# Kernel optimization log

Measured on AMD Instinct MI355X. Metric: run time of the kernel, lower is better.

## Reference

```python
import jax, jax.numpy as jnp
import numpy as np

N_HEAD = 16


def _rope_cos_sin(T, head_dim, dtype):
    inv_freq = 1.0 / (10000.0 ** (jnp.arange(0, head_dim, 2, dtype=jnp.float32) / head_dim))
    t = jnp.arange(T, dtype=jnp.float32)
    freqs = jnp.outer(t, inv_freq)  # [T, head_dim//2]
    return jnp.cos(freqs).astype(dtype), jnp.sin(freqs).astype(dtype)


def _apply_rope(x, cos, sin):
    # x: [B, H, T, D]; cos/sin: [T, D//2]
    x_even = x[..., ::2]
    x_odd = x[..., 1::2]
    c = cos[None, None, :, :]
    s = sin[None, None, :, :]
    out_even = x_even * c - x_odd * s
    out_odd = x_even * s + x_odd * c
    # interleave back: [..., D//2, 2] -> [..., D]
    return jnp.stack((out_even, out_odd), axis=-1).reshape(x.shape)


def setup_inputs() -> dict:
    key = jax.random.key(0)
    k1, k2, k3 = jax.random.split(key, 3)
    B, T, C = 2, 2048, 1024
    x = jax.random.normal(k1, (B, T, C), dtype=jnp.float32)
    w_qkv = jax.random.normal(k2, (C, 3 * C), dtype=jnp.float32) * (1.0 / np.sqrt(C))
    w_proj = jax.random.normal(k3, (C, C), dtype=jnp.float32) * (1.0 / np.sqrt(C))
    b_proj = jnp.zeros((C,), dtype=jnp.float32)
    return {"x": x, "w_qkv": w_qkv, "w_proj": w_proj, "b_proj": b_proj}


def reference(x, w_qkv, w_proj, b_proj):
    B, T, C = x.shape
    H = N_HEAD
    D = C // H
    qkv = x @ w_qkv  # [B, T, 3C]
    q, k, v = jnp.split(qkv, 3, axis=2)
    # [B, T, C] -> [B, H, T, D]
    q = q.reshape(B, T, H, D).transpose(0, 2, 1, 3)
    k = k.reshape(B, T, H, D).transpose(0, 2, 1, 3)
    v = v.reshape(B, T, H, D).transpose(0, 2, 1, 3)
    cos, sin = _rope_cos_sin(T, D, q.dtype)
    q = _apply_rope(q, cos, sin)
    k = _apply_rope(k, cos, sin)
    # causal SDPA
    scale = 1.0 / np.sqrt(D)
    att = jnp.einsum('bhqd,bhkd->bhqk', q, k) * scale
    causal = jnp.tril(jnp.ones((T, T), dtype=bool))
    att = jnp.where(causal[None, None, :, :], att, jnp.finfo(att.dtype).min)
    att = jax.nn.softmax(att, axis=-1)
    y = jnp.einsum('bhqk,bhkd->bhqd', att, v)  # [B, H, T, D]
    y = y.transpose(0, 2, 1, 3).reshape(B, T, C)
    return y @ w_proj + b_proj
```

## Files before the change

### kernel.cpp

```cpp
#include <hip/hip_runtime.h>
#include <math.h>

#define T_SEQ 2048
#define CDIM  1024
#define HEADS 16
#define DHEAD 64
#define BATCH 2
#define M_ROWS 4096
#define QSCALE 0.18033688011112042f

typedef unsigned short u16;
typedef unsigned int u32;
typedef __attribute__((ext_vector_type(8))) short bf16x8;
typedef __attribute__((ext_vector_type(4))) float f32x4;
typedef __attribute__((ext_vector_type(16))) float f32x16;

__device__ inline u16 f2bf(float f) {
    u32 u = __builtin_bit_cast(u32, f);
    u32 r = (u + 0x7fffu + ((u >> 16) & 1u)) >> 16;
    return (u16)r;
}

__device__ inline u32 cvtpk(float lo, float hi) {
    u32 r;
    asm("v_cvt_pk_bf16_f32 %0, %1, %2" : "=v"(r) : "v"(lo), "v"(hi));
    return r;
}

__device__ inline void permswap(u32& x, u32& y) {
    asm volatile("v_permlane32_swap_b32 %0, %1" : "+v"(x), "+v"(y));
}

__device__ inline float fexp2(float x) {
#if __has_builtin(__builtin_amdgcn_exp2f)
    return __builtin_amdgcn_exp2f(x);
#else
    float r; asm("v_exp_f32 %0, %1" : "=v"(r) : "v"(x)); return r;
#endif
}

__device__ inline void gload16(const void* g, void* l) {
    __builtin_amdgcn_global_load_lds(
        (const __attribute__((address_space(1))) void*)g,
        (__attribute__((address_space(3))) void*)l, 16, 0, 0);
}

__global__ void rope_table_kernel(float* __restrict__ cosT, float* __restrict__ sinT) {
    int idx = blockIdx.x * blockDim.x + threadIdx.x;
    if (idx >= T_SEQ * 32) return;
    int t = idx >> 5;
    int i = idx & 31;
    float expo = (2.0f * (float)i) / 64.0f;
    float inv = powf(10000.0f, -expo);
    float a = (float)t * inv;
    cosT[idx] = cosf(a);
    sinT[idx] = sinf(a);
}

__global__ __launch_bounds__(256)
void conv_bf16(const float* __restrict__ in, u16* __restrict__ out, int n8) {
    int i = blockIdx.x * blockDim.x + threadIdx.x;
    if (i >= n8) return;
    const float4* p = (const float4*)(in + (size_t)i * 8);
    float4 a = p[0], b = p[1];
    uint4 o;
    o.x = (u32)f2bf(a.x) | ((u32)f2bf(a.y) << 16);
    o.y = (u32)f2bf(a.z) | ((u32)f2bf(a.w) << 16);
    o.z = (u32)f2bf(b.x) | ((u32)f2bf(b.y) << 16);
    o.w = (u32)f2bf(b.z) | ((u32)f2bf(b.w) << 16);
    *(uint4*)(out + (size_t)i * 8) = o;
}

__global__ __launch_bounds__(256)
void convT64(const float* __restrict__ in, u16* __restrict__ out, int K, int N) {
    __shared__ float Ls[64][65];
    const int tid = threadIdx.x;
    const int k0 = blockIdx.y << 6, n0 = blockIdx.x << 6;
    const int r0 = tid >> 4, c4 = (tid & 15) << 2;
#pragma unroll
    for (int p = 0; p < 4; p++) {
        int r = r0 + (p << 4);
        float4 v = *(const float4*)&in[(size_t)(k0 + r) * N + n0 + c4];
        Ls[r][c4 + 0] = v.x; Ls[r][c4 + 1] = v.y;
        Ls[r][c4 + 2] = v.z; Ls[r][c4 + 3] = v.w;
    }
    __syncthreads();
    const int n = tid >> 2, kq = (tid & 3) << 4;
    u32 pk[8];
#pragma unroll
    for (int j = 0; j < 8; j++) {
        float lo = Ls[kq + 2 * j][n], hi = Ls[kq + 2 * j + 1][n];
        pk[j] = (u32)f2bf(lo) | ((u32)f2bf(hi) << 16);
    }
    u32* dst = (u32*)&out[(size_t)(n0 + n) * K + k0 + kq];
    ((uint4*)dst)[0] = make_uint4(pk[0], pk[1], pk[2], pk[3]);
    ((uint4*)dst)[1] = make_uint4(pk[4], pk[5], pk[6], pk[7]);
}

__global__ __launch_bounds__(256)
void transposeV(const u16* __restrict__ in, u16* __restrict__ out) {
    __shared__ u16 Ls[64][72];
    const int tid = threadIdx.x;
    const int bh = blockIdx.y;
    const int t0 = blockIdx.x << 6;
    const u16* src = in + ((size_t)bh << 17) + ((size_t)t0 << 6);
#pragma unroll
    for (int p = 0; p < 2; p++) {
        int L = tid + (p << 8);
        int t = L >> 3, c = L & 7;
        uint4 v = *(const uint4*)&src[(size_t)t * 64 + (c << 3)];
        *(uint4*)&Ls[t][c << 3] = v;
    }
    __syncthreads();
    const int d = tid >> 2, tq = (tid & 3) << 4;
    u32 pk[8];
#pragma unroll
    for (int j = 0; j < 8; j++) {
        u16 lo = Ls[tq + 2 * j][d], hi = Ls[tq + 2 * j + 1][d];
        pk[j] = (u32)lo | ((u32)hi << 16);
    }
    u16* dst = out + ((size_t)bh << 17) + ((size_t)d << 11) + t0 + tq;
    ((uint4*)dst)[0] = make_uint4(pk[0], pk[1], pk[2], pk[3]);
    ((uint4*)dst)[1] = make_uint4(pk[4], pk[5], pk[6], pk[7]);
}

template <int EPI>
__global__ __launch_bounds__(256)
void gemm_bf16(const u16* __restrict__ A, const u16* __restrict__ Bt,
               int N, int K,
               const float* __restrict__ bias, float* __restrict__ outF,
               u16* __restrict__ qOut, u16* __restrict__ kOut, u16* __restrict__ vOut,
               const float* __restrict__ cosT, const float* __restrict__ sinT) {
    __shared__ u16 Alds[2][128 * 32];
    __shared__ u16 Blds[2][128 * 32];
    const int tid = threadIdx.x;
    const int lane = tid & 63;
    const int w = tid >> 6;
    const int wr = w >> 1, wc = w & 1;
    const int g = lane >> 4, l15 = lane & 15;
    const int m0 = blockIdx.y * 128, n0 = blockIdx.x * 128;

    f32x4 acc[4][4];
#pragma unroll
    for (int m = 0; m < 4; m++)
#pragma unroll
        for (int n = 0; n < 4; n++)
#pragma unroll
            for (int e = 0; e < 4; e++) acc[m][n][e] = 0.f;

    int aoff[4], boff[4];
#pragma unroll
    for (int m = 0; m < 4; m++) {
        aoff[m] = ((wr << 6) + (m << 4) + l15) * 64 + (g << 4);
        boff[m] = ((wc << 6) + (m << 4) + l15) * 64 + (g << 4);
    }
    const int rowA0 = tid >> 2, kk0 = (tid & 3) << 3;

#define GSTAGE(BUF, K0)                                                          \
    {                                                                            \
        _Pragma("unroll") for (int pq = 0; pq < 2; pq++) {                       \
            int L = tid + (pq << 8);                                             \
            int row = rowA0 + (pq << 6);                                         \
            gload16(A + (size_t)(m0 + row) * K + (K0) + kk0, &Alds[BUF][0] + L * 8); \
            gload16(Bt + (size_t)(n0 + row) * K + (K0) + kk0, &Blds[BUF][0] + L * 8); \
        }                                                                        \
    }

    GSTAGE(0, 0);
    const int nt = K >> 5;
    int cur = 0;
    for (int t = 0; t < nt; t++) {
        if (t + 1 < nt) {
            GSTAGE(cur ^ 1, ((t + 1) << 5));
            asm volatile("s_waitcnt vmcnt(4)" ::: "memory");
        } else {
            asm volatile("s_waitcnt vmcnt(0)" ::: "memory");
        }
        __builtin_amdgcn_s_barrier();
        asm volatile("" ::: "memory");
        bf16x8 af[4], bfr[4];
#pragma unroll
        for (int m = 0; m < 4; m++) af[m] = *(const bf16x8*)((const char*)&Alds[cur][0] + aoff[m]);
#pragma unroll
        for (int n = 0; n < 4; n++) bfr[n] = *(const bf16x8*)((const char*)&Blds[cur][0] + boff[n]);
#pragma unroll
        for (int m = 0; m < 4; m++)
#pragma unroll
            for (int n = 0; n < 4; n++)
                acc[m][n] = __builtin_amdgcn_mfma_f32_16x16x32_bf16(af[m], bfr[n], acc[m][n], 0, 0, 0);
        asm volatile("" ::: "memory");
        __builtin_amdgcn_s_barrier();
        cur ^= 1;
    }
#undef GSTAGE

    if (EPI == 0) {
        const int sec = n0 >> 10;
#pragma unroll
        for (int m = 0; m < 4; m++) {
#pragma unroll
            for (int j = 0; j < 4; j++) {
                int t = m0 + (wr << 6) + (m << 4) + (g << 2) + j;
                int b = t >> 11, tt = t & 2047;
#pragma unroll
                for (int n = 0; n < 4; n++) {
                    int cc = (n0 + (wc << 6) + (n << 4) + l15) & 1023;
                    int h = cc >> 6, d = cc & 63;
                    float val = acc[m][n][j];
                    float o = val;
                    if (sec < 2) {
                        float partner = __shfl_xor(val, 1);
                        int i0 = d >> 1;
                        float c = cosT[tt * 32 + i0], s = sinT[tt * 32 + i0];
                        o = ((d & 1) == 0) ? (val * c - partner * s)
                                           : (partner * s + val * c);
                        if (sec == 0) o *= QSCALE;
                    }
                    size_t off = (((size_t)((b * 16 + h) * 2048 + tt)) << 6) + d;
                    u16* dst = (sec == 0) ? qOut : ((sec == 1) ? kOut : vOut);
                    dst[off] = f2bf(o);
                }
            }
        }
    } else {
#pragma unroll
        for (int m = 0; m < 4; m++) {
#pragma unroll
            for (int j = 0; j < 4; j++) {
                int t = m0 + (wr << 6) + (m << 4) + (g << 2) + j;
#pragma unroll
                for (int n = 0; n < 4; n++) {
                    int col = n0 + (wc << 6) + (n << 4) + l15;
                    outF[(size_t)t * N + col] = acc[m][n][j] + bias[col];
                }
            }
        }
    }
}

__device__ __forceinline__ void kv_stage2(const u16* Kb, const u16* Vtb,
                                          u16* Kl, u16* Vl, int tid, int k0) {
#pragma unroll
    for (int pp = 0; pp < 2; pp++) {
        int L = tid + (pp << 8);
        int row = L >> 3, c = L & 7;
        int cg = (c ^ (row & 7)) << 3;
        gload16(Kb + (((size_t)(k0 + row)) << 6) + cg, Kl + L * 8);
        gload16(Vtb + ((size_t)row << 11) + k0 + cg, Vl + L * 8);
    }
}

template <bool MASKED>
__device__ __forceinline__ void attn_step32(
    const bf16x8 (&qf)[4], f32x16 (&O)[2], float& MR, float& LR,
    const char* Kl, const char* Vl, const int (&foff)[2][4], int lim) {
    f32x16 st[2];
    __builtin_amdgcn_s_setprio(1);
#pragma unroll
    for (int s = 0; s < 2; s++) {
#pragma unroll
        for (int e = 0; e < 16; e++) st[s][e] = 0.f;
#pragma unroll
        for (int ks = 0; ks < 4; ks++) {
            bf16x8 kf = *(const bf16x8*)(Kl + foff[s][ks]);
            st[s] = __builtin_amdgcn_mfma_f32_32x32x16_bf16(kf, qf[ks], st[s], 0, 0, 0);
        }
    }
    __builtin_amdgcn_s_setprio(0);
    if (MASKED) {
#pragma unroll
        for (int s = 0; s < 2; s++) {
            const int ls = lim - (s << 5);
#pragma unroll
            for (int r = 0; r < 16; r++) {
                const int kvloc = (r & 3) + 8 * (r >> 2);
                if (kvloc > ls) st[s][r] = -1e30f;
            }
        }
    }
    float t8[8];
#pragma unroll
    for (int r = 0; r < 8; r++)
        t8[r] = fmaxf(fmaxf(st[0][r], st[0][r + 8]),
                      fmaxf(st[1][r], st[1][r + 8]));
    float m = fmaxf(fmaxf(fmaxf(t8[0], t8[4]), fmaxf(t8[1], t8[5])),
                    fmaxf(fmaxf(t8[2], t8[6]), fmaxf(t8[3], t8[7])));
    m = fmaxf(m, __shfl_xor(m, 32));
    float mn = fmaxf(MR, m);
    if (__ballot(m - MR > 10.f)) {
        float al = fexp2(MR - mn);
        MR = mn;
        LR *= al;
#pragma unroll
        for (int e = 0; e < 16; e++) { O[0][e] *= al; O[1][e] *= al; }
    }
    float s0 = 0.f, s1 = 0.f, s2 = 0.f, s3 = 0.f;
#pragma unroll
    for (int s = 0; s < 2; s++)
#pragma unroll
        for (int r = 0; r < 16; r++) {
            float pv = fexp2(st[s][r] - MR);
            st[s][r] = pv;
            if ((r & 3) == 0) s0 += pv;
            else if ((r & 3) == 1) s1 += pv;
            else if ((r & 3) == 2) s2 += pv;
            else s3 += pv;
        }
    float sum = (s0 + s1) + (s2 + s3);
    sum += __shfl_xor(sum, 32);
    LR += sum;
#pragma unroll
    for (int ks = 0; ks < 4; ks++) {
        const int sT = ks >> 1, b1 = (ks & 1) << 3;
        u32 a = cvtpk(st[sT][b1 + 0], st[sT][b1 + 1]);
        u32 b = cvtpk(st[sT][b1 + 2], st[sT][b1 + 3]);
        u32 c = cvtpk(st[sT][b1 + 4], st[sT][b1 + 5]);
        u32 d = cvtpk(st[sT][b1 + 6], st[sT][b1 + 7]);
        permswap(a, c);
        permswap(b, d);
        bf16x8 pf = __builtin_bit_cast(bf16x8, make_uint4(a, b, c, d));
        __builtin_amdgcn_s_setprio(1);
#pragma unroll
        for (int t2 = 0; t2 < 2; t2++) {
            bf16x8 vf = *(const bf16x8*)(Vl + foff[t2][ks]);
            O[t2] = __builtin_amdgcn_mfma_f32_32x32x16_bf16(vf, pf, O[t2], 0, 0, 0);
        }
        __builtin_amdgcn_s_setprio(0);
    }
}

__device__ __forceinline__ void attn_store32(
    const f32x16 (&O)[2], float LR, u16* __restrict__ Yg,
    int b, int hd, int q, int hl) {
    float inv = 1.0f / LR;
    size_t rowoff = (((size_t)(b * 2048 + q)) << 10) + (hd << 6);
#pragma unroll
    for (int t2 = 0; t2 < 2; t2++)
#pragma unroll
        for (int rg = 0; rg < 4; rg++) {
            int d0 = (rg << 3) + (hl << 2) + (t2 << 5);
            u32 lo = cvtpk(O[t2][4 * rg + 0] * inv, O[t2][4 * rg + 1] * inv);
            u32 hi = cvtpk(O[t2][4 * rg + 2] * inv, O[t2][4 * rg + 3] * inv);
            *(uint2*)&Yg[rowoff + d0] = make_uint2(lo, hi);
        }
}

__global__ __launch_bounds__(256)
void attn_mfma(const u16* __restrict__ Qg, const u16* __restrict__ Kg,
               const u16* __restrict__ Vtg, u16* __restrict__ Yg) {
    __shared__ u16 Ks[2][64 * 64];
    __shared__ u16 Vts[2][64 * 64];

    const int tid = threadIdx.x;
    const int lane = tid & 63;
    const int w = tid >> 6;
    const int l31 = lane & 31, hl = lane >> 5;
    const int bh = (int)blockIdx.x;
    const int Qi = (int)gridDim.y - 1 - (int)blockIdx.y;
    const int b = bh >> 4, hd = bh & 15;
    const int qbw = (Qi << 7) + (w << 5);
    const int q_lane = qbw + l31;
    const int nst = 2 * Qi + 2;

    const u16* Qb = Qg + ((size_t)bh << 17);
    const u16* Kb = Kg + ((size_t)bh << 17);
    const u16* Vtb = Vtg + ((size_t)bh << 17);

    int foff[2][4];
#pragma unroll
    for (int s = 0; s < 2; s++)
#pragma unroll
        for (int ks = 0; ks < 4; ks++) {
            int row = (s << 5) + l31;
            foff[s][ks] = row * 128 + (((hl + (ks << 1)) ^ (row & 7)) << 4);
        }

    bf16x8 qf[4];
#pragma unroll
    for (int ks = 0; ks < 4; ks++)
        qf[ks] = *(const bf16x8*)(Qb + (((size_t)q_lane) << 6) + (hl << 3) + (ks << 4));

    f32x16 O[2];
#pragma unroll
    for (int e = 0; e < 16; e++) { O[0][e] = 0.f; O[1][e] = 0.f; }
    float MR = -1e30f, LR = 0.f;

    kv_stage2(Kb, Vtb, &Ks[0][0], &Vts[0][0], tid, 0);
    int cur = 0;

    for (int kt = 0; kt < nst; kt++) {
        if (kt + 1 < nst) {
            kv_stage2(Kb, Vtb, &Ks[cur ^ 1][0], &Vts[cur ^ 1][0], tid, (kt + 1) << 6);
            asm volatile("s_waitcnt vmcnt(4)" ::: "memory");
        } else {
            asm volatile("s_waitcnt vmcnt(0)" ::: "memory");
        }
        __builtin_amdgcn_s_barrier();
        asm volatile("" ::: "memory");
        const int kv0 = kt << 6;
        if (kv0 <= qbw + 31) {
            if (qbw - kv0 >= 63) {
                attn_step32<false>(qf, O, MR, LR, (const char*)&Ks[cur][0],
                                   (const char*)&Vts[cur][0], foff, 0);
            } else {
                int lim = q_lane - kv0 - (hl << 2);
                attn_step32<true>(qf, O, MR, LR, (const char*)&Ks[cur][0],
                                  (const char*)&Vts[cur][0], foff, lim);
            }
        }
        asm volatile("" ::: "memory");
        __builtin_amdgcn_s_barrier();
        cur ^= 1;
    }
    attn_store32(O, LR, Yg, b, hd, q_lane, hl);
}

extern "C" void kernel_launch(void* const* d_in, const int* in_sizes, int n_in,
                              void* d_out, int out_size, void* d_ws, size_t ws_size,
                              hipStream_t stream) {
    const float* x      = (const float*)d_in[0];
    const float* w_qkv  = (const float*)d_in[1];
    const float* w_proj = (const float*)d_in[2];
    const float* b_proj = (const float*)d_in[3];
    float* out = (float*)d_out;

    const size_t SZ = (size_t)M_ROWS * CDIM;
    char* ws = (char*)d_ws;
    u16* xb     = (u16*)ws;                ws += SZ * 2;
    u16* wqkvT  = (u16*)ws;                ws += (size_t)3 * CDIM * CDIM * 2;
    u16* wprojT = (u16*)ws;                ws += (size_t)CDIM * CDIM * 2;
    u16* Qb     = (u16*)ws;                ws += SZ * 2;
    u16* Kb     = (u16*)ws;                ws += SZ * 2;
    u16* Vb     = (u16*)ws;                ws += SZ * 2;
    u16* Vt     = (u16*)ws;                ws += SZ * 2;
    u16* Yb     = (u16*)ws;                ws += SZ * 2;
    float* cosT = (float*)ws;              ws += (size_t)T_SEQ * 32 * 4;
    float* sinT = (float*)ws;              ws += (size_t)T_SEQ * 32 * 4;

    rope_table_kernel<<<dim3(256), dim3(256), 0, stream>>>(cosT, sinT);
    conv_bf16<<<dim3(2048), dim3(256), 0, stream>>>(x, xb, (int)(SZ / 8));
    convT64<<<dim3(48, 16), dim3(256), 0, stream>>>(w_qkv, wqkvT, CDIM, 3 * CDIM);
    convT64<<<dim3(16, 16), dim3(256), 0, stream>>>(w_proj, wprojT, CDIM, CDIM);

    gemm_bf16<0><<<dim3(24, 32), dim3(256), 0, stream>>>(
        xb, wqkvT, 3 * CDIM, CDIM, nullptr, nullptr, Qb, Kb, Vb, cosT, sinT);

    transposeV<<<dim3(32, 32), dim3(256), 0, stream>>>(Vb, Vt);

    attn_mfma<<<dim3(32, 16), dim3(256), 0, stream>>>(Qb, Kb, Vt, Yb);

    gemm_bf16<1><<<dim3(8, 32), dim3(256), 0, stream>>>(
        Yb, wprojT, CDIM, CDIM, b_proj, out, nullptr, nullptr, nullptr, nullptr, nullptr);
}
```

Measured before the change: 213.2 us.

## Move RoPE out of QKV GEMM epilogue into separate vectorized kernel

```diff
diff --git a/kernel.cpp b/kernel.cpp
--- a/kernel.cpp
+++ b/kernel.cpp
@@ -19,6 +19,11 @@
     u32 u = __builtin_bit_cast(u32, f);
     u32 r = (u + 0x7fffu + ((u >> 16) & 1u)) >> 16;
     return (u16)r;
+}
+
+__device__ inline float bf2f(u16 h) {
+    u32 u = ((u32)h) << 16;
+    return __builtin_bit_cast(float, u);
 }
 
 __device__ inline u32 cvtpk(float lo, float hi) {
@@ -98,17 +103,55 @@
 }
 
 __global__ __launch_bounds__(256)
-void transposeV(const u16* __restrict__ in, u16* __restrict__ out) {
+void ropeQK(const u16* __restrict__ qkv, u16* __restrict__ Qb, u16* __restrict__ Kb,
+            const float* __restrict__ cosT, const float* __restrict__ sinT) {
+    int L = blockIdx.x * 256 + threadIdx.x;
+    int m = L >> 8;
+    int col0 = (L & 255) << 3;
+    int sec = col0 >> 10;
+    int cc = col0 & 1023;
+    int h = cc >> 6, d0 = cc & 63;
+    int b = m >> 11, t = m & 2047;
+
+    uint4 v = *(const uint4*)&qkv[(size_t)m * 3072 + col0];
+    float e0 = bf2f((u16)v.x), o0 = bf2f((u16)(v.x >> 16));
+    float e1 = bf2f((u16)v.y), o1 = bf2f((u16)(v.y >> 16));
+    float e2 = bf2f((u16)v.z), o2 = bf2f((u16)(v.z >> 16));
+    float e3 = bf2f((u16)v.w), o3 = bf2f((u16)(v.w >> 16));
+
+    int i0 = d0 >> 1;
+    float4 c4v = *(const float4*)&cosT[t * 32 + i0];
+    float4 s4v = *(const float4*)&sinT[t * 32 + i0];
+
+    float re0 = e0 * c4v.x - o0 * s4v.x, ro0 = e0 * s4v.x + o0 * c4v.x;
+    float re1 = e1 * c4v.y - o1 * s4v.y, ro1 = e1 * s4v.y + o1 * c4v.y;
+    float re2 = e2 * c4v.z - o2 * s4v.z, ro2 = e2 * s4v.z + o2 * c4v.z;
+    float re3 = e3 * c4v.w - o3 * s4v.w, ro3 = e3 * s4v.w + o3 * c4v.w;
+
+    if (sec == 0) {
+        re0 *= QSCALE; ro0 *= QSCALE; re1 *= QSCALE; ro1 *= QSCALE;
+        re2 *= QSCALE; ro2 *= QSCALE; re3 *= QSCALE; ro3 *= QSCALE;
+    }
+    uint4 o;
+    o.x = cvtpk(re0, ro0); o.y = cvtpk(re1, ro1);
+    o.z = cvtpk(re2, ro2); o.w = cvtpk(re3, ro3);
+    u16* dst = (sec == 0) ? Qb : Kb;
+    *(uint4*)&dst[(((size_t)((b * 16 + h) * 2048 + t)) << 6) + d0] = o;
+}
+
+__global__ __launch_bounds__(256)
+void transposeV2(const u16* __restrict__ qkv, u16* __restrict__ out) {
     __shared__ u16 Ls[64][72];
     const int tid = threadIdx.x;
     const int bh = blockIdx.y;
+    const int b = bh >> 4, h = bh & 15;
     const int t0 = blockIdx.x << 6;
-    const u16* src = in + ((size_t)bh << 17) + ((size_t)t0 << 6);
+    const u16* src = qkv + (size_t)(b * 2048 + t0) * 3072 + 2048 + (h << 6);
 #pragma unroll
     for (int p = 0; p < 2; p++) {
         int L = tid + (p << 8);
         int t = L >> 3, c = L & 7;
-        uint4 v = *(const uint4*)&src[(size_t)t * 64 + (c << 3)];
+        uint4 v = *(const uint4*)&src[(size_t)t * 3072 + (c << 3)];
         *(uint4*)&Ls[t][c << 3] = v;
     }
     __syncthreads();
@@ -129,8 +172,7 @@
 void gemm_bf16(const u16* __restrict__ A, const u16* __restrict__ Bt,
                int N, int K,
                const float* __restrict__ bias, float* __restrict__ outF,
-               u16* __restrict__ qOut, u16* __restrict__ kOut, u16* __restrict__ vOut,
-               const float* __restrict__ cosT, const float* __restrict__ sinT) {
+               u16* __restrict__ outB) {
     __shared__ u16 Alds[2][128 * 32];
     __shared__ u16 Blds[2][128 * 32];
     const int tid = threadIdx.x;
@@ -195,30 +237,16 @@
 #undef GSTAGE
 
     if (EPI == 0) {
-        const int sec = n0 >> 10;
 #pragma unroll
         for (int m = 0; m < 4; m++) {
 #pragma unroll
             for (int j = 0; j < 4; j++) {
                 int t = m0 + (wr << 6) + (m << 4) + (g << 2) + j;
-                int b = t >> 11, tt = t & 2047;
+                u16* rowp = outB + (size_t)t * N;
 #pragma unroll
                 for (int n = 0; n < 4; n++) {
-                    int cc = (n0 + (wc << 6) + (n << 4) + l15) & 1023;
-                    int h = cc >> 6, d = cc & 63;
-                    float val = acc[m][n][j];
-                    float o = val;
-                    if (sec < 2) {
-                        float partner = __shfl_xor(val, 1);
-                        int i0 = d >> 1;
-                        float c = cosT[tt * 32 + i0], s = sinT[tt * 32 + i0];
-                        o = ((d & 1) == 0) ? (val * c - partner * s)
-                                           : (partner * s + val * c);
-                        if (sec == 0) o *= QSCALE;
-                    }
-                    size_t off = (((size_t)((b * 16 + h) * 2048 + tt)) << 6) + d;
-                    u16* dst = (sec == 0) ? qOut : ((sec == 1) ? kOut : vOut);
-                    dst[off] = f2bf(o);
+                    int col = n0 + (wc << 6) + (n << 4) + l15;
+                    rowp[col] = f2bf(acc[m][n][j]);
                 }
             }
         }
@@ -429,13 +457,13 @@
     u16* xb     = (u16*)ws;                ws += SZ * 2;
     u16* wqkvT  = (u16*)ws;                ws += (size_t)3 * CDIM * CDIM * 2;
     u16* wprojT = (u16*)ws;                ws += (size_t)CDIM * CDIM * 2;
+    u16* qkvb   = (u16*)ws;                ws += (size_t)M_ROWS * 3 * CDIM * 2;
     u16* Qb     = (u16*)ws;                ws += SZ * 2;
     u16* Kb     = (u16*)ws;                ws += SZ * 2;
-    u16* Vb     = (u16*)ws;                ws += SZ * 2;
     u16* Vt     = (u16*)ws;                ws += SZ * 2;
-    u16* Yb     = (u16*)ws;                ws += SZ * 2;
     float* cosT = (float*)ws;              ws += (size_t)T_SEQ * 32 * 4;
     float* sinT = (float*)ws;              ws += (size_t)T_SEQ * 32 * 4;
+    u16* Yb = qkvb;
 
     rope_table_kernel<<<dim3(256), dim3(256), 0, stream>>>(cosT, sinT);
     conv_bf16<<<dim3(2048), dim3(256), 0, stream>>>(x, xb, (int)(SZ / 8));
@@ -443,12 +471,13 @@
     convT64<<<dim3(16, 16), dim3(256), 0, stream>>>(w_proj, wprojT, CDIM, CDIM);
 
     gemm_bf16<0><<<dim3(24, 32), dim3(256), 0, stream>>>(
-        xb, wqkvT, 3 * CDIM, CDIM, nullptr, nullptr, Qb, Kb, Vb, cosT, sinT);
-
-    transposeV<<<dim3(32, 32), dim3(256), 0, stream>>>(Vb, Vt);
+        xb, wqkvT, 3 * CDIM, CDIM, nullptr, nullptr, qkvb);
+
+    ropeQK<<<dim3(4096), dim3(256), 0, stream>>>(qkvb, Qb, Kb, cosT, sinT);
+    transposeV2<<<dim3(32, 32), dim3(256), 0, stream>>>(qkvb, Vt);
 
     attn_mfma<<<dim3(32, 16), dim3(256), 0, stream>>>(Qb, Kb, Vt, Yb);
 
     gemm_bf16<1><<<dim3(8, 32), dim3(256), 0, stream>>>(
-        Yb, wprojT, CDIM, CDIM, b_proj, out, nullptr, nullptr, nullptr, nullptr, nullptr);
-}
+        Yb, wprojT, CDIM, CDIM, b_proj, out, nullptr);
+}
```

New measurement: 209.7 us. Within noise of the previous version (-1.6%).
